# Kernel optimization log

Measured on AMD Instinct MI355X. Metric: run time of the kernel, lower is better.

The kernel has to match this reference:

```python
import jax, jax.numpy as jnp
import numpy as np

H, D, DM, L, B = 16, 64, 1024, 256, 64
SCALE = 1.0 / np.sqrt(D)   # 1/sqrt(d_head)
CHUNK = 64
LN_EPS = 1e-5


def setup_inputs() -> dict:
    key = jax.random.key(0)
    k0, k1, k2, k3 = jax.random.split(key, 4)
    h = jax.random.normal(k0, (L, B, DM), jnp.float32)
    qkv_w = jax.random.normal(k1, (H * 4 * D, DM), jnp.float32) * 0.02
    o_w = jax.random.normal(k2, (DM, H * D), jnp.float32) * 0.02
    ln_gamma = jnp.ones((DM,), jnp.float32)
    ln_beta = jnp.zeros((DM,), jnp.float32)
    pi0 = jax.random.uniform(k3, (H, 256), jnp.float32)
    return {"h": h, "qkv_w": qkv_w, "o_w": o_w,
            "ln_gamma": ln_gamma, "ln_beta": ln_beta, "pi0": pi0}


def _phi(x):
    # elu(x) + 1, then sum-normalize over feature dim
    e = jax.nn.elu(x) + 1.0
    return e / e.sum(-1, keepdims=True)


def _fast_weight_sum(q, k, v):
    # q,k,v: [B,H,L,D]. out[t] = q_t @ W_t, W_t = sum_{s<=t} k_s v_s^T (inclusive).
    # Chunked-recurrent form: intra-chunk causal GEMM + inter-chunk carried state.
    Bb, Hh, Ll, Dd = q.shape
    nc = Ll // CHUNK
    rs = lambda x: x.reshape(Bb, Hh, nc, CHUNK, Dd).transpose(2, 0, 1, 3, 4)  # [nc,B,H,C,D]
    qc, kc, vc = rs(q), rs(k), rs(v)
    mask = jnp.tril(jnp.ones((CHUNK, CHUNK), q.dtype))  # inclusive causal

    def step(W, xs):
        qi, ki, vi = xs  # [B,H,C,D]
        scores = jnp.einsum('bhtd,bhsd->bhts', qi, ki) * mask
        out = jnp.einsum('bhts,bhsd->bhtd', scores, vi) \
            + jnp.einsum('bhtd,bhde->bhte', qi, W)
        W = W + jnp.einsum('bhsd,bhse->bhde', ki, vi)
        return W, out

    W0 = jnp.zeros((Bb, Hh, Dd, Dd), q.dtype)
    _, outs = jax.lax.scan(step, W0, (qc, kc, vc))  # outs: [nc,B,H,C,D]
    return outs.transpose(1, 2, 0, 3, 4).reshape(Bb, Hh, Ll, Dd)


def reference(h, qkv_w, o_w, ln_gamma, ln_beta, pi0):
    slen, bsz, _ = h.shape
    # qkv projection and head split (rbf2keys: q, k1, k2, v)
    qkv = (h @ qkv_w.T).reshape(slen, bsz, H, 4 * D)
    hq, hk1, hk2, hv = jnp.split(qkv, 4, axis=-1)       # each [L,B,H,D]
    perm = lambda x: x.transpose(1, 2, 0, 3)            # -> [B,H,L,D]
    hq, hk1, hk2, hv = perm(hq), perm(hk1), perm(hk2), perm(hv)

    hq = _phi(hq)
    hk1 = _phi(hk1)
    hk2 = _phi(hk2)

    out1 = _fast_weight_sum(hq, hk1, hv)
    out2 = _fast_weight_sum(hq, hk2, hv)

    # skip_attn_normalization=True path: pi0-gated mixture of the two memories
    p = jnp.clip(pi0, 0.0, 1.0)[None, :, :slen, None]   # [1,H,L,1]
    layer_out = SCALE * (out1 * p + out2 * (1.0 - p))   # [B,H,L,D]

    # [B,H,L,D] -> [L,B,H*D]
    layer_out = layer_out.transpose(0, 2, 1, 3).reshape(bsz, slen, H * D).transpose(1, 0, 2)
    attn_out = layer_out @ o_w.T                        # [L,B,DM]

    # post-LN residual (pre_lnorm=False)
    x = h + attn_out
    mu = x.mean(-1, keepdims=True)
    var = ((x - mu) ** 2).mean(-1, keepdims=True)
    return (x - mu) / jnp.sqrt(var + LN_EPS) * ln_gamma + ln_beta
```

## Files before the change

kernel.cpp:

```cpp
#include <hip/hip_runtime.h>
#include <type_traits>


typedef short v8s __attribute__((ext_vector_type(8)));
typedef float v4f __attribute__((ext_vector_type(4)));

__device__ __forceinline__ float bf2f(short s) {
    unsigned int u = ((unsigned int)(unsigned short)s) << 16;
    float f;
    __builtin_memcpy(&f, &u, 4);
    return f;
}
__device__ __forceinline__ short f2bf(float f) {
    unsigned int u;
    __builtin_memcpy(&u, &f, 4);
    u = u + 0x7fffu + ((u >> 16) & 1u);
    return (short)(u >> 16);
}

__device__ __forceinline__ void load_lds16(const short* g, short* l) {
    __builtin_amdgcn_global_load_lds((const __attribute__((address_space(1))) void*)g,
                                     (__attribute__((address_space(3))) void*)l, 16, 0, 0);
}

__global__ void __launch_bounds__(256)
cvt_bf16(const float* __restrict__ in, short* __restrict__ out, int n4) {
    int i = blockIdx.x * 256 + threadIdx.x;
    if (i >= n4) return;
    float4 v = ((const float4*)in)[i];
    short4 o;
    o.x = f2bf(v.x); o.y = f2bf(v.y); o.z = f2bf(v.z); o.w = f2bf(v.w);
    ((short4*)out)[i] = o;
}

template <typename OutT>
__global__ void __launch_bounds__(256)
gemm_nt(const short* __restrict__ A, const short* __restrict__ B,
        OutT* __restrict__ C, int M, int N, int K) {
    constexpr int BM = 128, BK = 32;
    __shared__ __align__(16) short sA[BM * BK];
    __shared__ __align__(16) short sB[BM * BK];
    const int tid = threadIdx.x;
    const int bm = blockIdx.x, bn = blockIdx.y;
    const int lane = tid & 63, w = tid >> 6;
    const int wy = w >> 1, wx = w & 1;
    const int lr = lane & 15, lq = lane >> 4;

    v4f acc[4][4] = {};

    const int srow = 32 * w + (lane >> 2);
    const int scol = (lane & 3) * 8;
    const short* gA0 = A + (long)(bm * BM + srow) * K + scol;
    const short* gB0 = B + (long)(bn * BM + srow) * K + scol;
    short* lA0 = sA + 32 * w * BK;
    short* lB0 = sB + 32 * w * BK;

    for (int kt = 0; kt < K; kt += BK) {
        __syncthreads();
        load_lds16(gA0 + kt, lA0);
        load_lds16(gA0 + 16 * K + kt, lA0 + 16 * BK);
        load_lds16(gB0 + kt, lB0);
        load_lds16(gB0 + 16 * K + kt, lB0 + 16 * BK);
        __syncthreads();

        v8s af[4], bfv[4];
#pragma unroll
        for (int i = 0; i < 4; i++)
            af[i] = *(const v8s*)&sA[(wy * 64 + i * 16 + lr) * BK + lq * 8];
#pragma unroll
        for (int j = 0; j < 4; j++)
            bfv[j] = *(const v8s*)&sB[(wx * 64 + j * 16 + lr) * BK + lq * 8];
#pragma unroll
        for (int i = 0; i < 4; i++)
#pragma unroll
            for (int j = 0; j < 4; j++)
                acc[i][j] = __builtin_amdgcn_mfma_f32_16x16x32_bf16(af[i], bfv[j], acc[i][j], 0, 0, 0);
    }
#pragma unroll
    for (int i = 0; i < 4; i++)
#pragma unroll
        for (int j = 0; j < 4; j++)
#pragma unroll
            for (int r = 0; r < 4; r++) {
                int row = bm * BM + wy * 64 + i * 16 + lq * 4 + r;
                int col = bn * BM + wx * 64 + j * 16 + lr;
                float v = acc[i][j][r];
                if constexpr (std::is_same_v<OutT, short>)
                    C[(long)row * N + col] = f2bf(v);
                else
                    C[(long)row * N + col] = v;
            }
}

#define SW(row, s) ((row) * 72 + ((((s) >> 3) ^ (((row) >> 4) & 7)) << 3) + ((s) & 7))

__global__ void __launch_bounds__(256)
fastweight(const short* __restrict__ qkv, short* __restrict__ out1, short* __restrict__ out2) {
    const int bid = blockIdx.x;
    const int mem = bid & 1, h = (bid >> 1) & 15, b = bid >> 5;
    const int tid = threadIdx.x;
    const int w = tid >> 6, lane = tid & 63;
    const int lq = lane >> 4, lr = lane & 15;
    __shared__ __align__(16) short sq[64 * 72];
    __shared__ __align__(16) short skS[64 * 72];
    __shared__ __align__(16) short skT[64 * 72];
    __shared__ __align__(16) short svT[64 * 72];
    __shared__ __align__(16) short sWT[64 * 72];
    short* outbuf = mem ? out2 : out1;
    const int koff = 64 + mem * 64;

    for (int i = tid; i < 64 * 36; i += 256) ((int*)sWT)[i] = 0;

    const int r = tid >> 2, seg = (tid & 3) * 16;

    v4f wacc[4] = {};

    for (int c = 0; c < 4; c++) {
        __syncthreads();
        const long gbase = ((long)((c * 64 + r) * 64 + b)) * 4096 + h * 256;
        {
            union { int4 v[2]; short s[16]; } u;
            u.v[0] = *(const int4*)(qkv + gbase + seg);
            u.v[1] = *(const int4*)(qkv + gbase + seg + 8);
            float f[16]; float ssum = 0.f;
#pragma unroll
            for (int i = 0; i < 16; i++) {
                float x = bf2f(u.s[i]);
                float e = x > 0.f ? x + 1.f : __expf(x);
                f[i] = e; ssum += e;
            }
            ssum += __shfl_xor(ssum, 1, 64);
            ssum += __shfl_xor(ssum, 2, 64);
            float inv = 1.f / ssum;
            union { int4 v[2]; short s[16]; } o;
#pragma unroll
            for (int i = 0; i < 16; i++) o.s[i] = f2bf(f[i] * inv);
            *(int4*)&sq[SW(r, seg)] = o.v[0];
            *(int4*)&sq[SW(r, seg + 8)] = o.v[1];
        }
        {
            union { int4 v[2]; short s[16]; } u;
            u.v[0] = *(const int4*)(qkv + gbase + koff + seg);
            u.v[1] = *(const int4*)(qkv + gbase + koff + seg + 8);
            float f[16]; float ssum = 0.f;
#pragma unroll
            for (int i = 0; i < 16; i++) {
                float x = bf2f(u.s[i]);
                float e = x > 0.f ? x + 1.f : __expf(x);
                f[i] = e; ssum += e;
            }
            ssum += __shfl_xor(ssum, 1, 64);
            ssum += __shfl_xor(ssum, 2, 64);
            float inv = 1.f / ssum;
            union { int4 v[2]; short s[16]; } o;
#pragma unroll
            for (int i = 0; i < 16; i++) o.s[i] = f2bf(f[i] * inv);
            *(int4*)&skS[SW(r, seg)] = o.v[0];
            *(int4*)&skS[SW(r, seg + 8)] = o.v[1];
#pragma unroll
            for (int i = 0; i < 16; i++) skT[SW(seg + i, r)] = o.s[i];
        }
        {
            union { int4 v[2]; short s[16]; } u;
            u.v[0] = *(const int4*)(qkv + gbase + 192 + seg);
            u.v[1] = *(const int4*)(qkv + gbase + 192 + seg + 8);
#pragma unroll
            for (int i = 0; i < 16; i++) svT[SW(seg + i, r)] = u.s[i];
        }
        __syncthreads();

        v8s qa0 = *(const v8s*)&sq[SW(16 * w + lr, lq * 8)];
        v8s qa1 = *(const v8s*)&sq[SW(16 * w + lr, 32 + lq * 8)];

        v4f sacc[4];
#pragma unroll
        for (int n = 0; n < 4; n++) {
            v8s b0 = *(const v8s*)&skS[SW(16 * n + lr, lq * 8)];
            v8s b1 = *(const v8s*)&skS[SW(16 * n + lr, 32 + lq * 8)];
            v4f t = {};
            t = __builtin_amdgcn_mfma_f32_16x16x32_bf16(qa0, b0, t, 0, 0, 0);
            t = __builtin_amdgcn_mfma_f32_16x16x32_bf16(qa1, b1, t, 0, 0, 0);
            sacc[n] = t;
        }
        __syncthreads();
#pragma unroll
        for (int n = 0; n < 4; n++)
#pragma unroll
            for (int rr = 0; rr < 4; rr++) {
                int t_ = 16 * w + lq * 4 + rr;
                int s_ = 16 * n + lr;
                skS[SW(t_, s_)] = f2bf(s_ <= t_ ? sacc[n][rr] : 0.f);
            }

        v8s sa0 = *(const v8s*)&skS[SW(16 * w + lr, lq * 8)];
        v8s sa1 = *(const v8s*)&skS[SW(16 * w + lr, 32 + lq * 8)];
        v4f oacc[4];
#pragma unroll
        for (int n = 0; n < 4; n++) {
            v8s vb0 = *(const v8s*)&svT[SW(16 * n + lr, lq * 8)];
            v8s vb1 = *(const v8s*)&svT[SW(16 * n + lr, 32 + lq * 8)];
            v8s wb0 = *(const v8s*)&sWT[SW(16 * n + lr, lq * 8)];
            v8s wb1 = *(const v8s*)&sWT[SW(16 * n + lr, 32 + lq * 8)];
            v4f t = {};
            t = __builtin_amdgcn_mfma_f32_16x16x32_bf16(sa0, vb0, t, 0, 0, 0);
            t = __builtin_amdgcn_mfma_f32_16x16x32_bf16(sa1, vb1, t, 0, 0, 0);
            t = __builtin_amdgcn_mfma_f32_16x16x32_bf16(qa0, wb0, t, 0, 0, 0);
            t = __builtin_amdgcn_mfma_f32_16x16x32_bf16(qa1, wb1, t, 0, 0, 0);
            oacc[n] = t;
        }
#pragma unroll
        for (int n = 0; n < 4; n++)
#pragma unroll
            for (int rr = 0; rr < 4; rr++) {
                int t_ = 16 * w + lq * 4 + rr;
                long o = ((long)((c * 64 + t_) * 64 + b)) * 1024 + h * 64 + 16 * n + lr;
                outbuf[o] = f2bf(oacc[n][rr]);
            }

        if (c < 3) {
            __syncthreads();
            v8s va0 = *(const v8s*)&svT[SW(16 * w + lr, lq * 8)];
            v8s va1 = *(const v8s*)&svT[SW(16 * w + lr, 32 + lq * 8)];
#pragma unroll
            for (int n = 0; n < 4; n++) {
                v8s kb0 = *(const v8s*)&skT[SW(16 * n + lr, lq * 8)];
                v8s kb1 = *(const v8s*)&skT[SW(16 * n + lr, 32 + lq * 8)];
                wacc[n] = __builtin_amdgcn_mfma_f32_16x16x32_bf16(va0, kb0, wacc[n], 0, 0, 0);
                wacc[n] = __builtin_amdgcn_mfma_f32_16x16x32_bf16(va1, kb1, wacc[n], 0, 0, 0);
            }
#pragma unroll
            for (int n = 0; n < 4; n++)
#pragma unroll
                for (int rr = 0; rr < 4; rr++)
                    sWT[SW(16 * w + lq * 4 + rr, 16 * n + lr)] = f2bf(wacc[n][rr]);
        }
    }
}

__global__ void __launch_bounds__(256)
mix_kernel(const short* __restrict__ l1, const short* __restrict__ l2,
           const float* __restrict__ pi0, short* __restrict__ outm) {
    long idx8 = ((long)blockIdx.x * 256 + threadIdx.x) * 8;
    int col = (int)(idx8 & 1023);
    int row = (int)(idx8 >> 10);
    int hh = col >> 6;
    int l = row >> 6;
    float p = pi0[hh * 256 + l];
    p = fminf(fmaxf(p, 0.f), 1.f);
    float q = 1.f - p;
    union { int4 v; short s[8]; } ua, ub, uo;
    ua.v = *(const int4*)(l1 + idx8);
    ub.v = *(const int4*)(l2 + idx8);
#pragma unroll
    for (int i = 0; i < 8; i++)
        uo.s[i] = f2bf(0.125f * (p * bf2f(ua.s[i]) + q * bf2f(ub.s[i])));
    *(int4*)(outm + idx8) = uo.v;
}

__global__ void __launch_bounds__(256)
ln_kernel(const float* __restrict__ h, const float* __restrict__ attn,
          const float* __restrict__ gamma, const float* __restrict__ beta,
          float* __restrict__ out) {
    const int row = blockIdx.x;
    const long base = (long)row * 1024;
    const int tid = threadIdx.x;
    float4 xh = ((const float4*)(h + base))[tid];
    float4 xa = ((const float4*)(attn + base))[tid];
    float4 x;
    x.x = xh.x + xa.x; x.y = xh.y + xa.y; x.z = xh.z + xa.z; x.w = xh.w + xa.w;
    float s = x.x + x.y + x.z + x.w;
    float s2 = x.x * x.x + x.y * x.y + x.z * x.z + x.w * x.w;
#pragma unroll
    for (int m = 32; m > 0; m >>= 1) {
        s += __shfl_xor(s, m, 64);
        s2 += __shfl_xor(s2, m, 64);
    }
    __shared__ float ps[4], ps2[4];
    int w = tid >> 6, lane = tid & 63;
    if (lane == 0) { ps[w] = s; ps2[w] = s2; }
    __syncthreads();
    s = ps[0] + ps[1] + ps[2] + ps[3];
    s2 = ps2[0] + ps2[1] + ps2[2] + ps2[3];
    float mu = s * (1.f / 1024.f);
    float var = s2 * (1.f / 1024.f) - mu * mu;
    float inv = rsqrtf(var + 1e-5f);
    float4 g = ((const float4*)gamma)[tid];
    float4 bb = ((const float4*)beta)[tid];
    float4 o;
    o.x = (x.x - mu) * inv * g.x + bb.x;
    o.y = (x.y - mu) * inv * g.y + bb.y;
    o.z = (x.z - mu) * inv * g.z + bb.z;
    o.w = (x.w - mu) * inv * g.w + bb.w;
    ((float4*)(out + base))[tid] = o;
}

extern "C" void kernel_launch(void* const* d_in, const int* in_sizes, int n_in,
                              void* d_out, int out_size, void* d_ws, size_t ws_size,
                              hipStream_t stream) {
    const float* h     = (const float*)d_in[0];
    const float* qkvw  = (const float*)d_in[1];
    const float* ow    = (const float*)d_in[2];
    const float* gamma = (const float*)d_in[3];
    const float* beta  = (const float*)d_in[4];
    const float* pi0   = (const float*)d_in[5];
    float* out = (float*)d_out;
    char* ws = (char*)d_ws;

    short* h_bf   = (short*)(ws);
    short* wq_bf  = (short*)(ws + 33554432);
    short* wo_bf  = (short*)(ws + 41943040);
    short* qkv_bf = (short*)(ws + 44040192);
    short* l1     = (short*)(ws + 178257920);
    short* l2     = (short*)(ws + 211812352);
    float* attnf  = (float*)(ws + 44040192);
    short* lmix   = h_bf;

    cvt_bf16<<<16384, 256, 0, stream>>>(h, h_bf, 16777216 / 4);
    cvt_bf16<<<4096, 256, 0, stream>>>(qkvw, wq_bf, 4194304 / 4);
    cvt_bf16<<<1024, 256, 0, stream>>>(ow, wo_bf, 1048576 / 4);

    gemm_nt<short><<<dim3(128, 32), 256, 0, stream>>>(h_bf, wq_bf, qkv_bf, 16384, 4096, 1024);

    fastweight<<<2048, 256, 0, stream>>>(qkv_bf, l1, l2);

    mix_kernel<<<8192, 256, 0, stream>>>(l1, l2, pi0, lmix);

    gemm_nt<float><<<dim3(128, 8), 256, 0, stream>>>(lmix, wo_bf, attnf, 16384, 1024, 1024);

    ln_kernel<<<16384, 256, 0, stream>>>(h, attnf, gamma, beta, out);
}
```

Baseline: 471.4 us.

## Fuse phi feature map into QKV GEMM epilogue and double GEMM K-tile with swizzle

Moves the elu+1 and sum-normalisation of q, k1 and k2 into the QKV projection GEMM epilogue. Each 64-column wave tile is one head's slice, and the row sum is reduced across lanes with shuffles. The fastweight kernel then loads already-normalised bf16 values and skips that recomputation. Separately, the GEMM K-tile grows from 32 to 64 with an XOR-swizzled LDS layout, meant to halve barrier count and avoid bank conflicts, at the cost of more LDS per block. Normalisation now runs on fp32 accumulators before bf16 rounding, so numerics shift slightly.

```diff
diff --git a/kernel.cpp b/kernel.cpp
--- a/kernel.cpp
+++ b/kernel.cpp
@@ -33,11 +33,11 @@
     ((short4*)out)[i] = o;
 }
 
-template <typename OutT>
+template <typename OutT, bool PHI>
 __global__ void __launch_bounds__(256)
 gemm_nt(const short* __restrict__ A, const short* __restrict__ B,
         OutT* __restrict__ C, int M, int N, int K) {
-    constexpr int BM = 128, BK = 32;
+    constexpr int BM = 128, BK = 64;
     __shared__ __align__(16) short sA[BM * BK];
     __shared__ __align__(16) short sB[BM * BK];
     const int tid = threadIdx.x;
@@ -48,48 +48,83 @@
 
     v4f acc[4][4] = {};
 
-    const int srow = 32 * w + (lane >> 2);
-    const int scol = (lane & 3) * 8;
-    const short* gA0 = A + (long)(bm * BM + srow) * K + scol;
-    const short* gB0 = B + (long)(bn * BM + srow) * K + scol;
+    const int sr = lane >> 3;
+    const int sg = (lane & 7) ^ sr;
+    const short* gA0 = A + (long)(bm * BM + 32 * w + sr) * K + sg * 8;
+    const short* gB0 = B + (long)(bn * BM + 32 * w + sr) * K + sg * 8;
     short* lA0 = sA + 32 * w * BK;
     short* lB0 = sB + 32 * w * BK;
 
+    const short* fA[2][4];
+    const short* fB[2][4];
+#pragma unroll
+    for (int half = 0; half < 2; half++)
+#pragma unroll
+        for (int i = 0; i < 4; i++) {
+            int rowA = wy * 64 + i * 16 + lr;
+            int rowB = wx * 64 + i * 16 + lr;
+            fA[half][i] = &sA[rowA * BK + (((half * 4 + lq) ^ (lr & 7)) * 8)];
+            fB[half][i] = &sB[rowB * BK + (((half * 4 + lq) ^ (lr & 7)) * 8)];
+        }
+
     for (int kt = 0; kt < K; kt += BK) {
         __syncthreads();
-        load_lds16(gA0 + kt, lA0);
-        load_lds16(gA0 + 16 * K + kt, lA0 + 16 * BK);
-        load_lds16(gB0 + kt, lB0);
-        load_lds16(gB0 + 16 * K + kt, lB0 + 16 * BK);
-        __syncthreads();
-
-        v8s af[4], bfv[4];
-#pragma unroll
-        for (int i = 0; i < 4; i++)
-            af[i] = *(const v8s*)&sA[(wy * 64 + i * 16 + lr) * BK + lq * 8];
-#pragma unroll
-        for (int j = 0; j < 4; j++)
-            bfv[j] = *(const v8s*)&sB[(wx * 64 + j * 16 + lr) * BK + lq * 8];
-#pragma unroll
-        for (int i = 0; i < 4; i++)
-#pragma unroll
-            for (int j = 0; j < 4; j++)
-                acc[i][j] = __builtin_amdgcn_mfma_f32_16x16x32_bf16(af[i], bfv[j], acc[i][j], 0, 0, 0);
+#pragma unroll
+        for (int j = 0; j < 4; j++) load_lds16(gA0 + 8 * j * K + kt, lA0 + 8 * j * BK);
+#pragma unroll
+        for (int j = 0; j < 4; j++) load_lds16(gB0 + 8 * j * K + kt, lB0 + 8 * j * BK);
+        __syncthreads();
+#pragma unroll
+        for (int half = 0; half < 2; half++) {
+            v8s af[4], bfv[4];
+#pragma unroll
+            for (int i = 0; i < 4; i++) af[i] = *(const v8s*)fA[half][i];
+#pragma unroll
+            for (int j = 0; j < 4; j++) bfv[j] = *(const v8s*)fB[half][j];
+#pragma unroll
+            for (int i = 0; i < 4; i++)
+#pragma unroll
+                for (int j = 0; j < 4; j++)
+                    acc[i][j] = __builtin_amdgcn_mfma_f32_16x16x32_bf16(af[i], bfv[j], acc[i][j], 0, 0, 0);
+        }
     }
+
+    const bool dophi = PHI && (((bn * 2 + wx) & 3) < 3);
 #pragma unroll
     for (int i = 0; i < 4; i++)
 #pragma unroll
-        for (int j = 0; j < 4; j++)
-#pragma unroll
-            for (int r = 0; r < 4; r++) {
-                int row = bm * BM + wy * 64 + i * 16 + lq * 4 + r;
+        for (int r = 0; r < 4; r++) {
+            float vv[4];
+#pragma unroll
+            for (int j = 0; j < 4; j++) vv[j] = acc[i][j][r];
+            if constexpr (PHI) {
+                if (dophi) {
+                    float s = 0.f;
+#pragma unroll
+                    for (int j = 0; j < 4; j++) {
+                        float x = vv[j];
+                        float e = x > 0.f ? x + 1.f : __expf(x);
+                        vv[j] = e; s += e;
+                    }
+                    s += __shfl_xor(s, 1, 64);
+                    s += __shfl_xor(s, 2, 64);
+                    s += __shfl_xor(s, 4, 64);
+                    s += __shfl_xor(s, 8, 64);
+                    float inv = 1.f / s;
+#pragma unroll
+                    for (int j = 0; j < 4; j++) vv[j] *= inv;
+                }
+            }
+            int row = bm * BM + wy * 64 + i * 16 + lq * 4 + r;
+#pragma unroll
+            for (int j = 0; j < 4; j++) {
                 int col = bn * BM + wx * 64 + j * 16 + lr;
-                float v = acc[i][j][r];
                 if constexpr (std::is_same_v<OutT, short>)
-                    C[(long)row * N + col] = f2bf(v);
+                    C[(long)row * N + col] = f2bf(vv[j]);
                 else
-                    C[(long)row * N + col] = v;
-            }
+                    C[(long)row * N + col] = vv[j];
+            }
+        }
 }
 
 #define SW(row, s) ((row) * 72 + ((((s) >> 3) ^ (((row) >> 4) & 7)) << 3) + ((s) & 7))
@@ -119,46 +154,19 @@
         __syncthreads();
         const long gbase = ((long)((c * 64 + r) * 64 + b)) * 4096 + h * 256;
         {
-            union { int4 v[2]; short s[16]; } u;
-            u.v[0] = *(const int4*)(qkv + gbase + seg);
-            u.v[1] = *(const int4*)(qkv + gbase + seg + 8);
-            float f[16]; float ssum = 0.f;
-#pragma unroll
-            for (int i = 0; i < 16; i++) {
-                float x = bf2f(u.s[i]);
-                float e = x > 0.f ? x + 1.f : __expf(x);
-                f[i] = e; ssum += e;
-            }
-            ssum += __shfl_xor(ssum, 1, 64);
-            ssum += __shfl_xor(ssum, 2, 64);
-            float inv = 1.f / ssum;
-            union { int4 v[2]; short s[16]; } o;
-#pragma unroll
-            for (int i = 0; i < 16; i++) o.s[i] = f2bf(f[i] * inv);
-            *(int4*)&sq[SW(r, seg)] = o.v[0];
-            *(int4*)&sq[SW(r, seg + 8)] = o.v[1];
+            int4 q0 = *(const int4*)(qkv + gbase + seg);
+            int4 q1 = *(const int4*)(qkv + gbase + seg + 8);
+            *(int4*)&sq[SW(r, seg)] = q0;
+            *(int4*)&sq[SW(r, seg + 8)] = q1;
         }
         {
             union { int4 v[2]; short s[16]; } u;
             u.v[0] = *(const int4*)(qkv + gbase + koff + seg);
             u.v[1] = *(const int4*)(qkv + gbase + koff + seg + 8);
-            float f[16]; float ssum = 0.f;
-#pragma unroll
-            for (int i = 0; i < 16; i++) {
-                float x = bf2f(u.s[i]);
-                float e = x > 0.f ? x + 1.f : __expf(x);
-                f[i] = e; ssum += e;
-            }
-            ssum += __shfl_xor(ssum, 1, 64);
-            ssum += __shfl_xor(ssum, 2, 64);
-            float inv = 1.f / ssum;
-            union { int4 v[2]; short s[16]; } o;
-#pragma unroll
-            for (int i = 0; i < 16; i++) o.s[i] = f2bf(f[i] * inv);
-            *(int4*)&skS[SW(r, seg)] = o.v[0];
-            *(int4*)&skS[SW(r, seg + 8)] = o.v[1];
-#pragma unroll
-            for (int i = 0; i < 16; i++) skT[SW(seg + i, r)] = o.s[i];
+            *(int4*)&skS[SW(r, seg)] = u.v[0];
+            *(int4*)&skS[SW(r, seg + 8)] = u.v[1];
+#pragma unroll
+            for (int i = 0; i < 16; i++) skT[SW(seg + i, r)] = u.s[i];
         }
         {
             union { int4 v[2]; short s[16]; } u;
@@ -319,13 +327,13 @@
     cvt_bf16<<<4096, 256, 0, stream>>>(qkvw, wq_bf, 4194304 / 4);
     cvt_bf16<<<1024, 256, 0, stream>>>(ow, wo_bf, 1048576 / 4);
 
-    gemm_nt<short><<<dim3(128, 32), 256, 0, stream>>>(h_bf, wq_bf, qkv_bf, 16384, 4096, 1024);
+    gemm_nt<short, true><<<dim3(128, 32), 256, 0, stream>>>(h_bf, wq_bf, qkv_bf, 16384, 4096, 1024);
 
     fastweight<<<2048, 256, 0, stream>>>(qkv_bf, l1, l2);
 
     mix_kernel<<<8192, 256, 0, stream>>>(l1, l2, pi0, lmix);
 
-    gemm_nt<float><<<dim3(128, 8), 256, 0, stream>>>(lmix, wo_bf, attnf, 16384, 1024, 1024);
+    gemm_nt<float, false><<<dim3(128, 8), 256, 0, stream>>>(lmix, wo_bf, attnf, 16384, 1024, 1024);
 
     ln_kernel<<<16384, 256, 0, stream>>>(h, attnf, gamma, beta, out);
 }
```

New measurement: 476.6 us. Within noise of the previous version (+1.1%).
